# Optimization experiments

Measured on AMD Instinct MI355X. Metric: run time of the kernel, lower is better.

Reference implementation:

```python
import jax, jax.numpy as jnp
import numpy as np

B, S, N, D, H, C = 64, 4, 4096, 1024, 16, 14
HD = D // H
EPS = 1e-5


def _ln(x, g, b):
    m = jnp.mean(x, axis=-1, keepdims=True)
    v = jnp.mean((x - m) ** 2, axis=-1, keepdims=True)
    return (x - m) * jax.lax.rsqrt(v + EPS) * g + b


def setup_inputs() -> dict:
    key = jax.random.key(0)
    ks = jax.random.split(key, 12)
    std = 0.02
    return {
        "cls_tok": jax.random.normal(ks[0], (B, D), jnp.float32),
        "storage": jax.random.normal(ks[1], (B, S, D), jnp.float32),
        "patches": jax.random.normal(ks[2], (B, N, D), jnp.float32),
        "query": jax.random.normal(ks[3], (1, 1, D), jnp.float32) * std,
        "ln_kv_g": jnp.ones((D,), jnp.float32),
        "ln_kv_b": jnp.zeros((D,), jnp.float32),
        "Wq": jax.random.normal(ks[4], (D, D), jnp.float32) / np.sqrt(D).astype(np.float32),
        "Wk": jax.random.normal(ks[5], (D, D), jnp.float32) / np.sqrt(D).astype(np.float32),
        "Wv": jax.random.normal(ks[6], (D, D), jnp.float32) / np.sqrt(D).astype(np.float32),
        "bq": jnp.zeros((D,), jnp.float32),
        "bk": jnp.zeros((D,), jnp.float32),
        "bv": jnp.zeros((D,), jnp.float32),
        "Wo": jax.random.normal(ks[7], (D, D), jnp.float32) / np.sqrt(D).astype(np.float32),
        "bo": jnp.zeros((D,), jnp.float32),
        "ln_out_g": jnp.ones((D,), jnp.float32),
        "ln_out_b": jnp.zeros((D,), jnp.float32),
        "Wp": jax.random.normal(ks[8], (C, D), jnp.float32) * std,
        "bp": jnp.zeros((C,), jnp.float32),
    }


def reference(cls_tok, storage, patches, query, ln_kv_g, ln_kv_b,
              Wq, Wk, Wv, bq, bk, bv, Wo, bo, ln_out_g, ln_out_b, Wp, bp):
    # tokens: (B, L, D) with L = 1 + S + N
    tokens = jnp.concatenate([cls_tok[:, None, :], storage, patches], axis=1)
    kv = _ln(tokens, ln_kv_g, ln_kv_b)
    b = tokens.shape[0]
    q = jnp.broadcast_to(query, (b, 1, D))
    # torch MultiheadAttention: separate q/k/v projections then scaled dot-product
    qp = (q @ Wq.T + bq).reshape(b, 1, H, HD)
    kp = (kv @ Wk.T + bk).reshape(b, -1, H, HD)
    vp = (kv @ Wv.T + bv).reshape(b, -1, H, HD)
    scale = 1.0 / np.sqrt(HD).astype(np.float32)
    scores = jnp.einsum('bqhd,bkhd->bhqk', qp, kp) * scale  # (B, H, 1, L)
    attn = jax.nn.softmax(scores, axis=-1)
    ctx = jnp.einsum('bhqk,bkhd->bqhd', attn, vp).reshape(b, 1, D)
    pooled = ctx[:, 0] @ Wo.T + bo          # out projection, (B, D)
    pooled = _ln(pooled, ln_out_g, ln_out_b)
    return pooled @ Wp.T + bp               # (B, num_labels)
```

## Files before the change

### kernel.cpp

```cpp
#include <hip/hip_runtime.h>
#include <hip/hip_bf16.h>

#define BB 64
#define DD 1024
#define HH 16
#define LL 4101
#define NCH 8
#define CHUNK 513
#define SCALE 0.125f
#define LN_EPS 1e-5f
#define RGS 4112

typedef float  f32x4 __attribute__((ext_vector_type(4)));
typedef short  s16x8 __attribute__((ext_vector_type(8)));
typedef unsigned int u32x4 __attribute__((ext_vector_type(4)));

#define WS_QVEC 0
#define WS_GU   1024
#define WS_G    17408
#define WS_BU   17424
#define WS_CB   17440
#define WS_PL   17456
#define WS_PM   25648
#define WS_PA   33840
#define WS_CTX  8422448
#define WS_POOL 8487984

__device__ __forceinline__ unsigned int pk2(float a, float b) {
    __hip_bfloat162 h = __float22bfloat162_rn(make_float2(a, b));
    unsigned int r;
    __builtin_memcpy(&r, &h, 4);
    return r;
}

__global__ void k_qvec(const float* __restrict__ query, const float* __restrict__ Wq,
                       const float* __restrict__ bq, float* __restrict__ qvec) {
    int j = blockIdx.x; int lane = threadIdx.x;
    const float4* wr = reinterpret_cast<const float4*>(Wq + (size_t)j * DD);
    const float4* qr = reinterpret_cast<const float4*>(query);
    float s = 0.f;
#pragma unroll
    for (int k = 0; k < 4; ++k) {
        float4 a = wr[k * 64 + lane];
        float4 q = qr[k * 64 + lane];
        s += a.x * q.x + a.y * q.y + a.z * q.z + a.w * q.w;
    }
#pragma unroll
    for (int m = 1; m < 64; m <<= 1) s += __shfl_xor(s, m, 64);
    if (lane == 0) qvec[j] = s + bq[j];
}

__global__ void k_u(const float* __restrict__ Wk, const float* __restrict__ qvec,
                    const float* __restrict__ g, const float* __restrict__ bln,
                    float* __restrict__ gu, float* __restrict__ Gv, float* __restrict__ Bu) {
    int h = blockIdx.x; int tid = threadIdx.x;
    int w = tid >> 6, lane = tid & 63;
    __shared__ float qs[64];
    __shared__ float red[8];
    if (tid < 64) qs[tid] = qvec[h * 64 + tid];
    __syncthreads();
    int d0 = tid * 4;
    float ax = 0.f, ay = 0.f, az = 0.f, aw = 0.f;
    for (int i = 0; i < 64; ++i) {
        float q = qs[i];
        float4 wv = *reinterpret_cast<const float4*>(&Wk[(size_t)(h * 64 + i) * DD + d0]);
        ax += q * wv.x; ay += q * wv.y; az += q * wv.z; aw += q * wv.w;
    }
    float4 g4 = *reinterpret_cast<const float4*>(&g[d0]);
    float4 b4 = *reinterpret_cast<const float4*>(&bln[d0]);
    float ux = ax * SCALE, uy = ay * SCALE, uz = az * SCALE, uw = aw * SCALE;
    float4 gu4 = make_float4(ux * g4.x, uy * g4.y, uz * g4.z, uw * g4.w);
    *reinterpret_cast<float4*>(&gu[(size_t)h * DD + d0]) = gu4;
    float Gp = gu4.x + gu4.y + gu4.z + gu4.w;
    float Bp = ux * b4.x + uy * b4.y + uz * b4.z + uw * b4.w;
#pragma unroll
    for (int m = 1; m < 64; m <<= 1) { Gp += __shfl_xor(Gp, m, 64); Bp += __shfl_xor(Bp, m, 64); }
    if (lane == 0) { red[2 * w] = Gp; red[2 * w + 1] = Bp; }
    __syncthreads();
    if (tid == 0) {
        Gv[h] = red[0] + red[2] + red[4] + red[6];
        Bu[h] = red[1] + red[3] + red[5] + red[7];
    }
}

__global__ void k_cq(const float* __restrict__ qvec, const float* __restrict__ bk,
                     const float* __restrict__ Bu, float* __restrict__ CB) {
    int h = threadIdx.x;
    if (h < HH) {
        float s = 0.f;
        for (int i = 0; i < 64; ++i) s += qvec[h * 64 + i] * bk[h * 64 + i];
        CB[h] = Bu[h] + s * SCALE;
    }
}

__global__ __launch_bounds__(256, 2) void k_main(
    const float* __restrict__ cls, const float* __restrict__ sto,
    const float* __restrict__ pat, const float* __restrict__ gu,
    const float* __restrict__ Gv, const float* __restrict__ CBv,
    float* __restrict__ pA, float* __restrict__ pl, float* __restrict__ pM) {

    __shared__ __align__(16) ushort Xlds[8 * RGS];
    __shared__ __align__(16) f32x4 csr[4][2][64];
    __shared__ __align__(16) float sstat[2][32][4];
    __shared__ __align__(16) ushort alds[512];
    __shared__ float2 mrs[32];

    const int blk = blockIdx.x;
    const int b = blk >> 3, ch = blk & 7;
    const int row0 = ch * CHUNK;
    const int rows = min(CHUNK, LL - row0);
    const int nt = (rows + 31) >> 5;
    const int tid = threadIdx.x;
    const int w = tid >> 6, lane = tid & 63;
    const int lm = lane & 15, lg = lane >> 4;

    s16x8 guf[8];
    {
        const float* gubase = gu + (size_t)lm * DD + w * 256 + lg * 8;
#pragma unroll
        for (int s = 0; s < 8; ++s) {
            const float* p = gubase + s * 32;
            u32x4 t;
#pragma unroll
            for (int j = 0; j < 4; ++j) t[j] = pk2(p[2 * j], p[2 * j + 1]);
            s16x8 f; __builtin_memcpy(&f, &t, 16);
            guf[s] = f;
        }
    }
    s16x8 ones;
#pragma unroll
    for (int j = 0; j < 8; ++j) ones[j] = (short)0x3F80;

    const float Gh = Gv[lm], CBh = CBv[lm];

    f32x4 acc[16];
#pragma unroll
    for (int i = 0; i < 16; ++i) acc[i] = (f32x4){0.f, 0.f, 0.f, 0.f};
    float lacc = 0.f, macc = 0.f;

    const int C0 = (lm >> 2) * RGS + w * 1024 + (lg >> 1) * 64 + (lm & 3) * 16 + (lg & 1) * 8;
    const int A1O = 4 * RGS;
    const int bbase = lg * 2 * RGS + w * 1024 + lm;
    const int aoff = lm * 32 + lg * 8;

    for (int t = 0; t < nt; ++t) {
#pragma unroll 2
        for (int rr = 0; rr < 8; ++rr) {
            int rl = w * 8 + rr;
            int rloc = t * 32 + rl;
            bool valid = rloc < rows;
            float4 v[4];
            if (valid) {
                int gr = row0 + rloc;
                const float* src;
                if (gr == 0)      src = cls + (size_t)b * DD;
                else if (gr <= 4) src = sto + ((size_t)b * 4 + (gr - 1)) * DD;
                else              src = pat + ((size_t)b * 4096 + (gr - 5)) * DD;
                const float4* s4 = reinterpret_cast<const float4*>(src);
#pragma unroll
                for (int it = 0; it < 4; ++it) v[it] = s4[it * 64 + lane];
            } else {
#pragma unroll
                for (int it = 0; it < 4; ++it) v[it] = make_float4(0.f, 0.f, 0.f, 0.f);
            }
#pragma unroll
            for (int it = 0; it < 4; ++it) {
                uint2 pk;
                pk.x = pk2(v[it].x, v[it].y);
                pk.y = pk2(v[it].z, v[it].w);
                int d0 = 4 * (it * 64 + lane);
                int elem = (rl >> 2) * RGS + (d0 >> 4) * 64 + ((rl & 3) << 4) + (d0 & 15);
                *reinterpret_cast<uint2*>(&Xlds[elem]) = pk;
            }
        }
        __syncthreads();

        {
            f32x4 c0 = {0.f,0.f,0.f,0.f}, c1 = {0.f,0.f,0.f,0.f};
            f32x4 q0 = {0.f,0.f,0.f,0.f}, q1 = {0.f,0.f,0.f,0.f};
            f32x4 m0 = {0.f,0.f,0.f,0.f}, m1 = {0.f,0.f,0.f,0.f};
#pragma unroll
            for (int s = 0; s < 8; ++s) {
                s16x8 a0 = *reinterpret_cast<const s16x8*>(&Xlds[C0 + s * 128]);
                s16x8 a1 = *reinterpret_cast<const s16x8*>(&Xlds[C0 + A1O + s * 128]);
                c0 = __builtin_amdgcn_mfma_f32_16x16x32_bf16(a0, guf[s], c0, 0, 0, 0);
                c1 = __builtin_amdgcn_mfma_f32_16x16x32_bf16(a1, guf[s], c1, 0, 0, 0);
                q0 = __builtin_amdgcn_mfma_f32_16x16x32_bf16(a0, a0,     q0, 0, 0, 0);
                q1 = __builtin_amdgcn_mfma_f32_16x16x32_bf16(a1, a1,     q1, 0, 0, 0);
                m0 = __builtin_amdgcn_mfma_f32_16x16x32_bf16(a0, ones,   m0, 0, 0, 0);
                m1 = __builtin_amdgcn_mfma_f32_16x16x32_bf16(a1, ones,   m1, 0, 0, 0);
            }
            csr[w][0][lane] = c0;
            csr[w][1][lane] = c1;
            if (lg == (lm >> 2)) {
                sstat[0][lm][w]      = q0[lm & 3];
                sstat[0][16 + lm][w] = q1[lm & 3];
            }
            if (lm == 0) {
#pragma unroll
                for (int i = 0; i < 4; ++i) {
                    sstat[1][lg * 4 + i][w]      = m0[i];
                    sstat[1][16 + lg * 4 + i][w] = m1[i];
                }
            }
        }
        __syncthreads();

        if (lane < 32) {
            f32x4 qv = *reinterpret_cast<const f32x4*>(&sstat[0][lane][0]);
            f32x4 mv = *reinterpret_cast<const f32x4*>(&sstat[1][lane][0]);
            float s2 = qv[0] + qv[1] + qv[2] + qv[3];
            float s1 = mv[0] + mv[1] + mv[2] + mv[3];
            float mean = s1 * (1.f / 1024.f);
            float var  = s2 * (1.f / 1024.f) - mean * mean;
            float rstd = rsqrtf(var + LN_EPS);
            mrs[lane] = make_float2(rstd, -mean * rstd);
        }
        asm volatile("s_waitcnt lgkmcnt(0)" ::: "memory");
        __builtin_amdgcn_sched_barrier(0);
        {
            f32x4 d0v = csr[0][0][lane], d1v = csr[0][1][lane];
#pragma unroll
            for (int wp = 1; wp < 4; ++wp) {
                f32x4 e0 = csr[wp][0][lane], e1 = csr[wp][1][lane];
                d0v += e0; d1v += e1;
            }
#pragma unroll
            for (int tt = 0; tt < 2; ++tt) {
                f32x4 dv = tt ? d1v : d0v;
                int rbase = tt * 16 + lg * 4;
                float al[4];
#pragma unroll
                for (int i = 0; i < 4; ++i) {
                    float2 mr = mrs[rbase + i];
                    float sc = dv[i] * mr.x + (mr.y * Gh + CBh);
                    bool vld = (t * 32 + rbase + i) < rows;
                    float p = vld ? __expf(sc) : 0.f;
                    lacc += p;
                    macc += p * mr.y;
                    al[i] = p * mr.x;
                }
                unsigned int qq0 = pk2(al[0], al[1]);
                unsigned int qq1 = pk2(al[2], al[3]);
                *reinterpret_cast<unsigned int*>(&alds[lm * 32 + rbase])     = qq0;
                *reinterpret_cast<unsigned int*>(&alds[lm * 32 + rbase + 2]) = qq1;
            }
        }
        asm volatile("s_waitcnt lgkmcnt(0)" ::: "memory");
        __builtin_amdgcn_sched_barrier(0);

        {
            s16x8 af = *reinterpret_cast<const s16x8*>(&alds[aoff]);
#pragma unroll
            for (int dt = 0; dt < 16; ++dt) {
                s16x8 bfrag;
#pragma unroll
                for (int j = 0; j < 8; ++j) {
                    int e = bbase + dt * 64 + ((j & 3) << 4) + (j >> 2) * RGS;
                    bfrag[j] = (short)Xlds[e];
                }
                acc[dt] = __builtin_amdgcn_mfma_f32_16x16x32_bf16(af, bfrag, acc[dt], 0, 0, 0);
            }
        }
        __syncthreads();
    }

    size_t pabase = ((size_t)blk << 14);
#pragma unroll
    for (int dt = 0; dt < 16; ++dt) {
#pragma unroll
        for (int i = 0; i < 4; ++i) {
            int h = lg * 4 + i;
            pA[pabase + ((size_t)h << 10) + w * 256 + dt * 16 + lm] = acc[dt][i];
        }
    }
    if (w == 0) {
        lacc += __shfl_xor(lacc, 16, 64); lacc += __shfl_xor(lacc, 32, 64);
        macc += __shfl_xor(macc, 16, 64); macc += __shfl_xor(macc, 32, 64);
        if (lane < 16) {
            pl[blk * 16 + lane] = lacc;
            pM[blk * 16 + lane] = -macc;
        }
    }
}

__global__ void k_comb(float* __restrict__ pA, const float* __restrict__ pl,
                       const float* __restrict__ pM, const float* __restrict__ g,
                       const float* __restrict__ bln) {
    int blk = blockIdx.x; int b = blk >> 4; int h = blk & 15; int tid = threadIdx.x;
    float l = 0.f, M = 0.f;
#pragma unroll
    for (int ch = 0; ch < NCH; ++ch) {
        l += pl[(b * NCH + ch) * 16 + h];
        M += pM[(b * NCH + ch) * 16 + h];
    }
    float inv = 1.f / l;
    float4 s = make_float4(0.f, 0.f, 0.f, 0.f);
#pragma unroll
    for (int ch = 0; ch < NCH; ++ch) {
        const float4* p4 = reinterpret_cast<const float4*>(
            pA + (((size_t)(b * NCH + ch) * 16 + h) << 10));
        float4 v = p4[tid];
        s.x += v.x; s.y += v.y; s.z += v.z; s.w += v.w;
    }
    float4 g4 = *reinterpret_cast<const float4*>(&g[tid * 4]);
    float4 b4 = *reinterpret_cast<const float4*>(&bln[tid * 4]);
    float4 o;
    o.x = g4.x * (s.x - M) * inv + b4.x;
    o.y = g4.y * (s.y - M) * inv + b4.y;
    o.z = g4.z * (s.z - M) * inv + b4.z;
    o.w = g4.w * (s.w - M) * inv + b4.w;
    float4* dst = reinterpret_cast<float4*>(pA + (((size_t)(b * NCH) * 16 + h) << 10));
    dst[tid] = o;
}

__global__ void k_ctx(const float* __restrict__ Wv, const float* __restrict__ bv,
                      const float* __restrict__ pA, float* __restrict__ ctx) {
    int j = blockIdx.x; int h = j >> 6;
    int w = threadIdx.x >> 6, lane = threadIdx.x & 63;
    const float4* wr = reinterpret_cast<const float4*>(Wv + (size_t)j * DD);
    float4 wv[4];
#pragma unroll
    for (int k = 0; k < 4; ++k) wv[k] = wr[k * 64 + lane];
    float bvj = bv[j];
    for (int bb2 = w * 16; bb2 < w * 16 + 16; ++bb2) {
        const float4* sr = reinterpret_cast<const float4*>(
            pA + (((size_t)(bb2 * NCH) * 16 + h) << 10));
        float s = 0.f;
#pragma unroll
        for (int k = 0; k < 4; ++k) {
            float4 v = sr[k * 64 + lane];
            s += wv[k].x * v.x + wv[k].y * v.y + wv[k].z * v.z + wv[k].w * v.w;
        }
#pragma unroll
        for (int m = 1; m < 64; m <<= 1) s += __shfl_xor(s, m, 64);
        if (lane == 0) ctx[(size_t)bb2 * DD + j] = s + bvj;
    }
}

__global__ void k_pool(const float* __restrict__ Wo, const float* __restrict__ bo,
                       const float* __restrict__ ctx, float* __restrict__ pooled) {
    int j = blockIdx.x;
    int w = threadIdx.x >> 6, lane = threadIdx.x & 63;
    const float4* wr = reinterpret_cast<const float4*>(Wo + (size_t)j * DD);
    float4 wv[4];
#pragma unroll
    for (int k = 0; k < 4; ++k) wv[k] = wr[k * 64 + lane];
    float boj = bo[j];
    for (int bb2 = w * 16; bb2 < w * 16 + 16; ++bb2) {
        const float4* cr4 = reinterpret_cast<const float4*>(ctx + (size_t)bb2 * DD);
        float s = 0.f;
#pragma unroll
        for (int k = 0; k < 4; ++k) {
            float4 v = cr4[k * 64 + lane];
            s += wv[k].x * v.x + wv[k].y * v.y + wv[k].z * v.z + wv[k].w * v.w;
        }
#pragma unroll
        for (int m = 1; m < 64; m <<= 1) s += __shfl_xor(s, m, 64);
        if (lane == 0) pooled[(size_t)bb2 * DD + j] = s + boj;
    }
}

__global__ void k_head(const float* __restrict__ pooled, const float* __restrict__ g2,
                       const float* __restrict__ b2, const float* __restrict__ Wp,
                       const float* __restrict__ bp, float* __restrict__ out) {
    int b = blockIdx.x; int tid = threadIdx.x;
    __shared__ float pln[DD];
    __shared__ float red[8];
    const float4* pr = reinterpret_cast<const float4*>(pooled + (size_t)b * DD);
    float4 v = pr[tid];
    float s1 = v.x + v.y + v.z + v.w;
    float s2 = v.x * v.x + v.y * v.y + v.z * v.z + v.w * v.w;
#pragma unroll
    for (int m = 1; m < 64; m <<= 1) { s1 += __shfl_xor(s1, m, 64); s2 += __shfl_xor(s2, m, 64); }
    int w = tid >> 6, lane = tid & 63;
    if (lane == 0) { red[2 * w] = s1; red[2 * w + 1] = s2; }
    __syncthreads();
    s1 = red[0] + red[2] + red[4] + red[6];
    s2 = red[1] + red[3] + red[5] + red[7];
    float mean = s1 * (1.f / 1024.f);
    float var  = s2 * (1.f / 1024.f) - mean * mean;
    float rstd = rsqrtf(var + LN_EPS);
    int d0 = tid * 4;
    pln[d0 + 0] = (v.x - mean) * rstd * g2[d0 + 0] + b2[d0 + 0];
    pln[d0 + 1] = (v.y - mean) * rstd * g2[d0 + 1] + b2[d0 + 1];
    pln[d0 + 2] = (v.z - mean) * rstd * g2[d0 + 2] + b2[d0 + 2];
    pln[d0 + 3] = (v.w - mean) * rstd * g2[d0 + 3] + b2[d0 + 3];
    __syncthreads();
    int q = tid & 15, c = tid >> 4;
    if (c < 14) {
        float s = 0.f;
#pragma unroll 8
        for (int i = 0; i < 64; ++i) {
            int d = i * 16 + q;
            s += pln[d] * Wp[c * DD + d];
        }
#pragma unroll
        for (int m = 1; m < 16; m <<= 1) s += __shfl_xor(s, m, 64);
        if (q == 0) out[b * 14 + c] = s + bp[c];
    }
}

extern "C" void kernel_launch(void* const* d_in, const int* in_sizes, int n_in,
                              void* d_out, int out_size, void* d_ws, size_t ws_size,
                              hipStream_t stream) {
    const float* cls   = (const float*)d_in[0];
    const float* sto   = (const float*)d_in[1];
    const float* pat   = (const float*)d_in[2];
    const float* query = (const float*)d_in[3];
    const float* g     = (const float*)d_in[4];
    const float* bln   = (const float*)d_in[5];
    const float* Wq    = (const float*)d_in[6];
    const float* Wk    = (const float*)d_in[7];
    const float* Wv    = (const float*)d_in[8];
    const float* bq    = (const float*)d_in[9];
    const float* bk    = (const float*)d_in[10];
    const float* bv    = (const float*)d_in[11];
    const float* Wo    = (const float*)d_in[12];
    const float* bo    = (const float*)d_in[13];
    const float* g2    = (const float*)d_in[14];
    const float* b2    = (const float*)d_in[15];
    const float* Wp    = (const float*)d_in[16];
    const float* bp    = (const float*)d_in[17];

    float* ws     = (float*)d_ws;
    float* qvec   = ws + WS_QVEC;
    float* gu     = ws + WS_GU;
    float* Gv     = ws + WS_G;
    float* Bu     = ws + WS_BU;
    float* CB     = ws + WS_CB;
    float* pl     = ws + WS_PL;
    float* pM     = ws + WS_PM;
    float* pA     = ws + WS_PA;
    float* ctx    = ws + WS_CTX;
    float* pooled = ws + WS_POOL;
    float* out    = (float*)d_out;

    hipLaunchKernelGGL(k_qvec, dim3(1024), dim3(64), 0, stream, query, Wq, bq, qvec);
    hipLaunchKernelGGL(k_u,    dim3(16),   dim3(256), 0, stream, Wk, qvec, g, bln, gu, Gv, Bu);
    hipLaunchKernelGGL(k_cq,   dim3(1),    dim3(64), 0, stream, qvec, bk, Bu, CB);
    hipLaunchKernelGGL(k_main, dim3(BB * NCH), dim3(256), 0, stream,
                       cls, sto, pat, gu, Gv, CB, pA, pl, pM);
    hipLaunchKernelGGL(k_comb, dim3(BB * HH), dim3(256), 0, stream, pA, pl, pM, g, bln);
    hipLaunchKernelGGL(k_ctx,  dim3(1024), dim3(256), 0, stream, Wv, bv, pA, ctx);
    hipLaunchKernelGGL(k_pool, dim3(1024), dim3(256), 0, stream, Wo, bo, ctx, pooled);
    hipLaunchKernelGGL(k_head, dim3(64),   dim3(256), 0, stream, pooled, g2, b2, Wp, bp, out);
}
```

Measured before the change: 254.9 us.

## Fuse query projection into k_u, split across 64 blocks, store partials in bf16

The q-projection kernel is merged into k_u, which now runs 64 blocks (4 per head) instead of 16, and partial G/B sums are reduced in k_cq. That removes one launch and raises parallelism in the setup stage. The per-chunk attention partials written by k_main are stored as bf16 instead of fp32, halving the partial-buffer write and read traffic in k_main and k_comb. k_comb now writes combined results to a separate sbar buffer. Storing the partials in bf16 reduces the precision of the accumulated attention-weighted sums.

```diff
diff --git a/kernel.cpp b/kernel.cpp
--- a/kernel.cpp
+++ b/kernel.cpp
@@ -19,12 +19,14 @@
 #define WS_GU   1024
 #define WS_G    17408
 #define WS_BU   17424
-#define WS_CB   17440
-#define WS_PL   17456
-#define WS_PM   25648
-#define WS_PA   33840
-#define WS_CTX  8422448
-#define WS_POOL 8487984
+#define WS_BP   17488
+#define WS_CB   17552
+#define WS_PL   17568
+#define WS_PM   25760
+#define WS_PA   33952
+#define WS_SBAR 4228256
+#define WS_CTX  5276832
+#define WS_POOL 5342368
 
 __device__ __forceinline__ unsigned int pk2(float a, float b) {
     __hip_bfloat162 h = __float22bfloat162_rn(make_float2(a, b));
@@ -33,63 +35,70 @@
     return r;
 }
 
-__global__ void k_qvec(const float* __restrict__ query, const float* __restrict__ Wq,
-                       const float* __restrict__ bq, float* __restrict__ qvec) {
-    int j = blockIdx.x; int lane = threadIdx.x;
-    const float4* wr = reinterpret_cast<const float4*>(Wq + (size_t)j * DD);
-    const float4* qr = reinterpret_cast<const float4*>(query);
-    float s = 0.f;
-#pragma unroll
-    for (int k = 0; k < 4; ++k) {
-        float4 a = wr[k * 64 + lane];
-        float4 q = qr[k * 64 + lane];
-        s += a.x * q.x + a.y * q.y + a.z * q.z + a.w * q.w;
-    }
-#pragma unroll
-    for (int m = 1; m < 64; m <<= 1) s += __shfl_xor(s, m, 64);
-    if (lane == 0) qvec[j] = s + bq[j];
-}
-
-__global__ void k_u(const float* __restrict__ Wk, const float* __restrict__ qvec,
+__device__ __forceinline__ float bf2f(unsigned short u) {
+    unsigned int x = ((unsigned int)u) << 16;
+    float f;
+    __builtin_memcpy(&f, &x, 4);
+    return f;
+}
+
+__global__ void k_u(const float* __restrict__ query, const float* __restrict__ Wq,
+                    const float* __restrict__ bq, const float* __restrict__ Wk,
                     const float* __restrict__ g, const float* __restrict__ bln,
-                    float* __restrict__ gu, float* __restrict__ Gv, float* __restrict__ Bu) {
-    int h = blockIdx.x; int tid = threadIdx.x;
+                    float* __restrict__ qvec, float* __restrict__ gu,
+                    float* __restrict__ Gp, float* __restrict__ Bp) {
+    int h = blockIdx.x >> 2, q = blockIdx.x & 3;
+    int tid = threadIdx.x;
     int w = tid >> 6, lane = tid & 63;
     __shared__ float qs[64];
     __shared__ float red[8];
-    if (tid < 64) qs[tid] = qvec[h * 64 + tid];
+    {
+        int r = tid >> 2, part = tid & 3;
+        const float4* wr = reinterpret_cast<const float4*>(
+            Wq + (size_t)(h * 64 + r) * DD + part * 256);
+        const float4* qr = reinterpret_cast<const float4*>(query + part * 256);
+        float s = 0.f;
+#pragma unroll 8
+        for (int k = 0; k < 64; ++k) {
+            float4 a = wr[k];
+            float4 qq = qr[k];
+            s += a.x * qq.x + a.y * qq.y + a.z * qq.z + a.w * qq.w;
+        }
+        s += __shfl_xor(s, 1, 64);
+        s += __shfl_xor(s, 2, 64);
+        if (part == 0) qs[r] = s + bq[h * 64 + r];
+    }
     __syncthreads();
-    int d0 = tid * 4;
-    float ax = 0.f, ay = 0.f, az = 0.f, aw = 0.f;
-    for (int i = 0; i < 64; ++i) {
-        float q = qs[i];
-        float4 wv = *reinterpret_cast<const float4*>(&Wk[(size_t)(h * 64 + i) * DD + d0]);
-        ax += q * wv.x; ay += q * wv.y; az += q * wv.z; aw += q * wv.w;
-    }
-    float4 g4 = *reinterpret_cast<const float4*>(&g[d0]);
-    float4 b4 = *reinterpret_cast<const float4*>(&bln[d0]);
-    float ux = ax * SCALE, uy = ay * SCALE, uz = az * SCALE, uw = aw * SCALE;
-    float4 gu4 = make_float4(ux * g4.x, uy * g4.y, uz * g4.z, uw * g4.w);
-    *reinterpret_cast<float4*>(&gu[(size_t)h * DD + d0]) = gu4;
-    float Gp = gu4.x + gu4.y + gu4.z + gu4.w;
-    float Bp = ux * b4.x + uy * b4.y + uz * b4.z + uw * b4.w;
-#pragma unroll
-    for (int m = 1; m < 64; m <<= 1) { Gp += __shfl_xor(Gp, m, 64); Bp += __shfl_xor(Bp, m, 64); }
-    if (lane == 0) { red[2 * w] = Gp; red[2 * w + 1] = Bp; }
+    int d = q * 256 + tid;
+    float a = 0.f;
+#pragma unroll 8
+    for (int i = 0; i < 64; ++i) a += qs[i] * Wk[(size_t)(h * 64 + i) * DD + d];
+    float u = a * SCALE;
+    float guv = u * g[d];
+    gu[(size_t)h * DD + d] = guv;
+    float Gv_ = guv, Bv_ = u * bln[d];
+#pragma unroll
+    for (int m = 1; m < 64; m <<= 1) { Gv_ += __shfl_xor(Gv_, m, 64); Bv_ += __shfl_xor(Bv_, m, 64); }
+    if (lane == 0) { red[2 * w] = Gv_; red[2 * w + 1] = Bv_; }
     __syncthreads();
     if (tid == 0) {
-        Gv[h] = red[0] + red[2] + red[4] + red[6];
-        Bu[h] = red[1] + red[3] + red[5] + red[7];
-    }
+        Gp[h * 4 + q] = red[0] + red[2] + red[4] + red[6];
+        Bp[h * 4 + q] = red[1] + red[3] + red[5] + red[7];
+    }
+    if (q == 0 && tid < 64) qvec[h * 64 + tid] = qs[tid];
 }
 
 __global__ void k_cq(const float* __restrict__ qvec, const float* __restrict__ bk,
-                     const float* __restrict__ Bu, float* __restrict__ CB) {
+                     const float* __restrict__ Gp, const float* __restrict__ Bp,
+                     float* __restrict__ Gv, float* __restrict__ CB) {
     int h = threadIdx.x;
     if (h < HH) {
+        float G = Gp[h * 4] + Gp[h * 4 + 1] + Gp[h * 4 + 2] + Gp[h * 4 + 3];
+        float Bu = Bp[h * 4] + Bp[h * 4 + 1] + Bp[h * 4 + 2] + Bp[h * 4 + 3];
         float s = 0.f;
         for (int i = 0; i < 64; ++i) s += qvec[h * 64 + i] * bk[h * 64 + i];
-        CB[h] = Bu[h] + s * SCALE;
+        Gv[h] = G;
+        CB[h] = Bu + s * SCALE;
     }
 }
 
@@ -97,7 +106,7 @@
     const float* __restrict__ cls, const float* __restrict__ sto,
     const float* __restrict__ pat, const float* __restrict__ gu,
     const float* __restrict__ Gv, const float* __restrict__ CBv,
-    float* __restrict__ pA, float* __restrict__ pl, float* __restrict__ pM) {
+    ushort* __restrict__ pAb, float* __restrict__ pl, float* __restrict__ pM) {
 
     __shared__ __align__(16) ushort Xlds[8 * RGS];
     __shared__ __align__(16) f32x4 csr[4][2][64];
@@ -271,7 +280,8 @@
 #pragma unroll
         for (int i = 0; i < 4; ++i) {
             int h = lg * 4 + i;
-            pA[pabase + ((size_t)h << 10) + w * 256 + dt * 16 + lm] = acc[dt][i];
+            pAb[pabase + ((size_t)h << 10) + w * 256 + dt * 16 + lm] =
+                (ushort)(pk2(acc[dt][i], 0.f) & 0xffffu);
         }
     }
     if (w == 0) {
@@ -284,9 +294,9 @@
     }
 }
 
-__global__ void k_comb(float* __restrict__ pA, const float* __restrict__ pl,
+__global__ void k_comb(const ushort* __restrict__ pAb, const float* __restrict__ pl,
                        const float* __restrict__ pM, const float* __restrict__ g,
-                       const float* __restrict__ bln) {
+                       const float* __restrict__ bln, float* __restrict__ sbar) {
     int blk = blockIdx.x; int b = blk >> 4; int h = blk & 15; int tid = threadIdx.x;
     float l = 0.f, M = 0.f;
 #pragma unroll
@@ -298,10 +308,13 @@
     float4 s = make_float4(0.f, 0.f, 0.f, 0.f);
 #pragma unroll
     for (int ch = 0; ch < NCH; ++ch) {
-        const float4* p4 = reinterpret_cast<const float4*>(
-            pA + (((size_t)(b * NCH + ch) * 16 + h) << 10));
-        float4 v = p4[tid];
-        s.x += v.x; s.y += v.y; s.z += v.z; s.w += v.w;
+        const uint2* p2 = reinterpret_cast<const uint2*>(
+            pAb + (((size_t)(b * NCH + ch) * 16 + h) << 10));
+        uint2 v = p2[tid];
+        s.x += bf2f((unsigned short)(v.x & 0xffffu));
+        s.y += bf2f((unsigned short)(v.x >> 16));
+        s.z += bf2f((unsigned short)(v.y & 0xffffu));
+        s.w += bf2f((unsigned short)(v.y >> 16));
     }
     float4 g4 = *reinterpret_cast<const float4*>(&g[tid * 4]);
     float4 b4 = *reinterpret_cast<const float4*>(&bln[tid * 4]);
@@ -310,12 +323,12 @@
     o.y = g4.y * (s.y - M) * inv + b4.y;
     o.z = g4.z * (s.z - M) * inv + b4.z;
     o.w = g4.w * (s.w - M) * inv + b4.w;
-    float4* dst = reinterpret_cast<float4*>(pA + (((size_t)(b * NCH) * 16 + h) << 10));
+    float4* dst = reinterpret_cast<float4*>(sbar + (((size_t)(b * HH) + h) << 10));
     dst[tid] = o;
 }
 
 __global__ void k_ctx(const float* __restrict__ Wv, const float* __restrict__ bv,
-                      const float* __restrict__ pA, float* __restrict__ ctx) {
+                      const float* __restrict__ sbar, float* __restrict__ ctx) {
     int j = blockIdx.x; int h = j >> 6;
     int w = threadIdx.x >> 6, lane = threadIdx.x & 63;
     const float4* wr = reinterpret_cast<const float4*>(Wv + (size_t)j * DD);
@@ -325,7 +338,7 @@
     float bvj = bv[j];
     for (int bb2 = w * 16; bb2 < w * 16 + 16; ++bb2) {
         const float4* sr = reinterpret_cast<const float4*>(
-            pA + (((size_t)(bb2 * NCH) * 16 + h) << 10));
+            sbar + (((size_t)(bb2 * HH) + h) << 10));
         float s = 0.f;
 #pragma unroll
         for (int k = 0; k < 4; ++k) {
@@ -427,22 +440,24 @@
     float* qvec   = ws + WS_QVEC;
     float* gu     = ws + WS_GU;
     float* Gv     = ws + WS_G;
-    float* Bu     = ws + WS_BU;
+    float* Gp     = ws + WS_BU;
+    float* Bp     = ws + WS_BP;
     float* CB     = ws + WS_CB;
     float* pl     = ws + WS_PL;
     float* pM     = ws + WS_PM;
-    float* pA     = ws + WS_PA;
+    ushort* pAb   = (ushort*)(ws + WS_PA);
+    float* sbar   = ws + WS_SBAR;
     float* ctx    = ws + WS_CTX;
     float* pooled = ws + WS_POOL;
     float* out    = (float*)d_out;
 
-    hipLaunchKernelGGL(k_qvec, dim3(1024), dim3(64), 0, stream, query, Wq, bq, qvec);
-    hipLaunchKernelGGL(k_u,    dim3(16),   dim3(256), 0, stream, Wk, qvec, g, bln, gu, Gv, Bu);
-    hipLaunchKernelGGL(k_cq,   dim3(1),    dim3(64), 0, stream, qvec, bk, Bu, CB);
+    hipLaunchKernelGGL(k_u,    dim3(64),   dim3(256), 0, stream,
+                       query, Wq, bq, Wk, g, bln, qvec, gu, Gp, Bp);
+    hipLaunchKernelGGL(k_cq,   dim3(1),    dim3(64), 0, stream, qvec, bk, Gp, Bp, Gv, CB);
     hipLaunchKernelGGL(k_main, dim3(BB * NCH), dim3(256), 0, stream,
-                       cls, sto, pat, gu, Gv, CB, pA, pl, pM);
-    hipLaunchKernelGGL(k_comb, dim3(BB * HH), dim3(256), 0, stream, pA, pl, pM, g, bln);
-    hipLaunchKernelGGL(k_ctx,  dim3(1024), dim3(256), 0, stream, Wv, bv, pA, ctx);
+                       cls, sto, pat, gu, Gv, CB, pAb, pl, pM);
+    hipLaunchKernelGGL(k_comb, dim3(BB * HH), dim3(256), 0, stream, pAb, pl, pM, g, bln, sbar);
+    hipLaunchKernelGGL(k_ctx,  dim3(1024), dim3(256), 0, stream, Wv, bv, sbar, ctx);
     hipLaunchKernelGGL(k_pool, dim3(1024), dim3(256), 0, stream, Wo, bo, ctx, pooled);
     hipLaunchKernelGGL(k_head, dim3(64),   dim3(256), 0, stream, pooled, g2, b2, Wp, bp, out);
 }
```

Result: no change. 259.6 us (+1.9%).
